# Performance work log

Hardware: AMD Instinct MI355X
Metric: run time of the kernel (lower is better)

## Reference

```python
import math
import jax, jax.numpy as jnp
import numpy as np

B, IMG, CIN = 32, 32, 4
PATCH, HIDDEN, DEPTH, HEADS, MLP = 2, 768, 12, 12, 3072
FREQ, NUM_CLASSES = 256, 1000
GRID = IMG // PATCH
N = GRID * GRID
OUT = PATCH * PATCH * CIN


def _pos_embed(dim, length):
    # faithful port of get_2d_sincos_pos_embed
    g = int(math.sqrt(length))
    grid = np.stack(np.meshgrid(np.arange(g, dtype=np.float32),
                                np.arange(g, dtype=np.float32), indexing='ij')).reshape(2, -1)
    def emb1d(d, pos):
        omega = 1.0 / 10000.0 ** (np.arange(d // 2, dtype=np.float32) / (d / 2.0))
        out = np.einsum('m,d->md', pos, omega)
        return np.concatenate([np.sin(out), np.cos(out)], axis=1)
    pe = np.concatenate([emb1d(dim // 2, grid[0]), emb1d(dim // 2, grid[1])], axis=1)
    return jnp.asarray(pe[None], dtype=jnp.float32)  # [1, N, dim]


def _ln(x):
    # LayerNorm(elementwise_affine=False), eps=1e-5, biased variance
    m = jnp.mean(x, axis=-1, keepdims=True)
    v = jnp.var(x, axis=-1, keepdims=True)
    return (x - m) * jax.lax.rsqrt(v + 1e-5)


def setup_inputs() -> dict:
    key = jax.random.key(0)
    ks = jax.random.split(key, 20)
    w = lambda k, shape: jax.random.normal(k, shape, jnp.float32) * 0.02
    z = lambda *shape: jnp.zeros(shape, jnp.float32)
    return {
        'x': jax.random.normal(ks[0], (B, IMG, IMG, CIN), jnp.float32),
        't': jax.random.uniform(ks[1], (B,), jnp.float32) * 1000.0,
        'y': jax.random.randint(ks[2], (B,), 0, NUM_CLASSES + 1),
        'patch_w': w(ks[3], (PATCH * PATCH * CIN, HIDDEN)), 'patch_b': z(HIDDEN),
        't_w1': w(ks[4], (FREQ, HIDDEN)), 't_b1': z(HIDDEN),
        't_w2': w(ks[5], (HIDDEN, HIDDEN)), 't_b2': z(HIDDEN),
        'label_emb': w(ks[6], (NUM_CLASSES + 1, HIDDEN)),
        'ada_w': w(ks[7], (DEPTH, HIDDEN, 6 * HIDDEN)), 'ada_b': z(DEPTH, 6 * HIDDEN),
        'q_w': w(ks[8], (DEPTH, HIDDEN, HIDDEN)), 'q_b': z(DEPTH, HIDDEN),
        'k_w': w(ks[9], (DEPTH, HIDDEN, HIDDEN)), 'k_b': z(DEPTH, HIDDEN),
        'v_w': w(ks[10], (DEPTH, HIDDEN, HIDDEN)), 'v_b': z(DEPTH, HIDDEN),
        'o_w': w(ks[11], (DEPTH, HIDDEN, HIDDEN)), 'o_b': z(DEPTH, HIDDEN),
        'fc1_w': w(ks[12], (DEPTH, HIDDEN, MLP)), 'fc1_b': z(DEPTH, MLP),
        'fc2_w': w(ks[13], (DEPTH, MLP, HIDDEN)), 'fc2_b': z(DEPTH, HIDDEN),
        'fin_ada_w': w(ks[14], (HIDDEN, 2 * HIDDEN)), 'fin_ada_b': z(2 * HIDDEN),
        'fin_w': w(ks[15], (HIDDEN, OUT)), 'fin_b': z(OUT),
    }


def reference(x, t, y, patch_w, patch_b, t_w1, t_b1, t_w2, t_b2, label_emb,
              ada_w, ada_b, q_w, q_b, k_w, k_b, v_w, v_b, o_w, o_b,
              fc1_w, fc1_b, fc2_w, fc2_b, fin_ada_w, fin_ada_b, fin_w, fin_b):
    Bx = x.shape[0]
    dh = HIDDEN // HEADS
    # patch embed (conv k=p, stride=p == per-patch linear)
    patches = x.reshape(Bx, GRID, PATCH, GRID, PATCH, CIN)
    patches = patches.transpose(0, 1, 3, 2, 4, 5).reshape(Bx, N, PATCH * PATCH * CIN)
    h = patches @ patch_w + patch_b + _pos_embed(HIDDEN, N)
    # timestep embedding: [cos, sin] order
    half = FREQ // 2
    freqs = jnp.exp(-math.log(10000.0) * jnp.arange(half, dtype=jnp.float32) / half)
    args = t.astype(jnp.float32)[:, None] * freqs[None]
    temb = jnp.concatenate([jnp.cos(args), jnp.sin(args)], axis=-1)
    temb = jax.nn.silu(temb @ t_w1 + t_b1) @ t_w2 + t_b2
    c_act = jax.nn.silu(temb + label_emb[y])  # silu applied inside each block on c

    def block(hx, p):
        aw, ab, qw, qb, kw, kb, vw, vb, ow, ob, f1w, f1b, f2w, f2b = p
        ada = c_act @ aw + ab
        sh_m, sc_m, g_m, sh_p, sc_p, g_p = jnp.split(ada, 6, axis=-1)
        xn = _ln(hx) * (1.0 + sc_m[:, None]) + sh_m[:, None]
        q = ((xn @ qw + qb).reshape(Bx, N, HEADS, dh)) / math.sqrt(3.0)
        k = (xn @ kw + kb).reshape(Bx, N, HEADS, dh)
        v = (xn @ vw + vb).reshape(Bx, N, HEADS, dh)
        attn = jax.nn.softmax(jnp.einsum('bqhc,bkhc->bhqk', q, k).astype(jnp.float32), axis=-1)
        yv = jnp.einsum('bhqk,bkhc->bqhc', attn, v).reshape(Bx, N, HIDDEN)
        hx = hx + g_m[:, None] * (yv @ ow + ob)
        xn2 = _ln(hx) * (1.0 + sc_p[:, None]) + sh_p[:, None]
        mlp = jax.nn.gelu(xn2 @ f1w + f1b, approximate=False) @ f2w + f2b
        hx = hx + g_p[:, None] * mlp
        return hx, None

    h, _ = jax.lax.scan(block, h, (ada_w, ada_b, q_w, q_b, k_w, k_b, v_w, v_b,
                                   o_w, o_b, fc1_w, fc1_b, fc2_w, fc2_b))
    # final layer
    fada = c_act @ fin_ada_w + fin_ada_b
    sh, sc = jnp.split(fada, 2, axis=-1)
    out = (_ln(h) * (1.0 + sc[:, None]) + sh[:, None]) @ fin_w + fin_b
    return out  # [B, N, patch*patch*out_channels]
```

## Files before the change

kernel.cpp:

```cpp
#include <hip/hip_runtime.h>
#include <hip/hip_bf16.h>


typedef short  s16x8 __attribute__((ext_vector_type(8)));
typedef float  f32x4 __attribute__((ext_vector_type(4)));

__device__ __forceinline__ float bf2f(unsigned short u) {
    union { unsigned int i; float f; } v; v.i = ((unsigned int)u) << 16; return v.f;
}
__device__ __forceinline__ unsigned short f2bf(float f) {
    union { float f; unsigned int i; } v; v.f = f;
    unsigned int r = (v.i + 0x7FFFu + ((v.i >> 16) & 1u)) >> 16;
    return (unsigned short)r;
}
__device__ __forceinline__ float silu(float v) { return v / (1.f + __expf(-v)); }

__device__ __forceinline__ void gload16(const void* gptr, void* lptr) {
    __builtin_amdgcn_global_load_lds(
        (const __attribute__((address_space(1))) unsigned int*)gptr,
        (__attribute__((address_space(3))) unsigned int*)lptr,
        16, 0, 0);
}

#define ROWS 8192
#define HID  768
#define MLPD 3072
#define ADA_LD 4608

__global__ __launch_bounds__(256) void ada_init(const float* __restrict__ ada_b,
                                                const float* __restrict__ fada_b,
                                                const float* __restrict__ t_b1,
                                                const float* __restrict__ t_b2,
                                                const float* __restrict__ lemb,
                                                const int* __restrict__ y,
                                                float* __restrict__ ada_all,
                                                float* __restrict__ fada,
                                                float* __restrict__ z1,
                                                float* __restrict__ z2)
{
    const int bid = blockIdx.x, tid = threadIdx.x;
    if (bid >= 222) {
        const int col = (bid - 222) * 256 + tid;
        const float b1v = t_b1[col], b2v = t_b2[col];
        for (int r = 0; r < 32; ++r) {
            z1[(size_t)r * HID + col] = b1v;
            z2[(size_t)r * HID + col] = b2v + lemb[(size_t)y[r] * HID + col];
        }
        return;
    }
    const float* Bv; float* Out; int ldw, colb;
    if (bid < 216) {
        const int l = bid / 18; colb = (bid % 18) * 256;
        Bv = ada_b + (size_t)l * ADA_LD; Out = ada_all + (size_t)l * 32 * ADA_LD; ldw = ADA_LD;
    } else {
        colb = (bid - 216) * 256;
        Bv = fada_b; Out = fada; ldw = 1536;
    }
    const int col = colb + tid;
    const float bb = Bv[col];
    #pragma unroll
    for (int r = 0; r < 32; ++r) Out[(size_t)r * ldw + col] = bb;
}

__global__ __launch_bounds__(256) void temb1_k(const float* __restrict__ t,
                                               const float* __restrict__ w1,
                                               float* __restrict__ z1)
{
    __shared__ float tin[128];
    const int b = blockIdx.x, cc = blockIdx.y, kc = blockIdx.z, tid = threadIdx.x;
    const int k0 = kc * 128;
    if (tid < 128) {
        const int k = k0 + tid, j = k & 127;
        const float fr = __expf((float)j * (-9.210340371976184f / 128.f));
        const float a = t[b] * fr;
        tin[tid] = (k < 128) ? cosf(a) : sinf(a);
    }
    __syncthreads();
    const int col = cc * 256 + tid;
    float acc = 0.f;
    #pragma unroll 8
    for (int kk = 0; kk < 128; ++kk) acc += tin[kk] * w1[(size_t)(k0 + kk) * HID + col];
    atomicAdd(&z1[(size_t)b * HID + col], acc);
}

__global__ __launch_bounds__(256) void temb2_k(const float* __restrict__ z1,
                                               const float* __restrict__ w2,
                                               float* __restrict__ z2)
{
    __shared__ float tin[192];
    const int b = blockIdx.x, cc = blockIdx.y, kc = blockIdx.z, tid = threadIdx.x;
    const int k0 = kc * 192;
    if (tid < 192) tin[tid] = silu(z1[(size_t)b * HID + k0 + tid]);
    __syncthreads();
    const int col = cc * 256 + tid;
    float acc = 0.f;
    #pragma unroll 8
    for (int kk = 0; kk < 192; ++kk) acc += tin[kk] * w2[(size_t)(k0 + kk) * HID + col];
    atomicAdd(&z2[(size_t)b * HID + col], acc);
}

__global__ __launch_bounds__(64) void ada_gemm2(const float* __restrict__ z2,
                                                const float* __restrict__ ada_w,
                                                const float* __restrict__ fada_w,
                                                float* __restrict__ ada_all,
                                                float* __restrict__ fada)
{
    const int bx = blockIdx.x, kc = blockIdx.y, tid = threadIdx.x;
    const float* W; float* Out; int ldw, colb;
    if (bx < 216) {
        const int l = bx / 18; colb = (bx % 18) * 256;
        W = ada_w + (size_t)l * HID * ADA_LD; Out = ada_all + (size_t)l * 32 * ADA_LD; ldw = ADA_LD;
    } else {
        colb = (bx - 216) * 256;
        W = fada_w; Out = fada; ldw = 1536;
    }
    const int k0 = kc * 96;
    __shared__ float cs_[32][96];
    for (int i = tid; i < 32 * 96; i += 64)
        cs_[i / 96][i % 96] = silu(z2[(size_t)(i / 96) * HID + k0 + (i % 96)]);
    __syncthreads();
    float acc[4][32];
    #pragma unroll
    for (int j = 0; j < 4; ++j)
        #pragma unroll
        for (int r = 0; r < 32; ++r) acc[j][r] = 0.f;
    #pragma unroll 1
    for (int kk = 0; kk < 96; kk += 4) {
        float wv[4][4];
        #pragma unroll
        for (int i = 0; i < 4; ++i) {
            const float* Wr = W + (size_t)(k0 + kk + i) * ldw + colb + tid;
            #pragma unroll
            for (int j = 0; j < 4; ++j) wv[j][i] = Wr[64 * j];
        }
        #pragma unroll
        for (int r = 0; r < 32; ++r) {
            const float4 cv = *(const float4*)&cs_[r][kk];
            #pragma unroll
            for (int j = 0; j < 4; ++j)
                acc[j][r] += cv.x * wv[j][0] + cv.y * wv[j][1] + cv.z * wv[j][2] + cv.w * wv[j][3];
        }
    }
    #pragma unroll
    for (int j = 0; j < 4; ++j)
        #pragma unroll
        for (int r = 0; r < 32; ++r)
            atomicAdd(&Out[(size_t)r * ldw + colb + tid + 64 * j], acc[j][r]);
}

__global__ __launch_bounds__(256) void patch_embed(const float* __restrict__ x,
                                                   const float* __restrict__ pw,
                                                   const float* __restrict__ pb,
                                                   float* __restrict__ h)
{
    const int row = blockIdx.x;
    const int b = row >> 8, n = row & 255;
    const int gi = n >> 4, gj = n & 15;
    const int tid = threadIdx.x;
    __shared__ float pv[16];
    if (tid < 16) {
        const int pr = tid >> 3, pc = (tid >> 2) & 1, ci = tid & 3;
        pv[tid] = x[((size_t)(b * 32 + gi * 2 + pr) * 32 + (gj * 2 + pc)) * 4 + ci];
    }
    __syncthreads();
    #pragma unroll
    for (int cc = 0; cc < 3; ++cc) {
        const int col = cc * 256 + tid;
        float acc = pb[col];
        #pragma unroll
        for (int i = 0; i < 16; ++i) acc += pv[i] * pw[(size_t)i * HID + col];
        const int d4 = (col < 384) ? col : col - 384;
        const int pos = (col < 384) ? gi : gj;
        const float kf = (float)(d4 < 192 ? d4 : d4 - 192);
        const float om = __expf(kf * (-9.210340371976184f / 192.f));
        const float a = (float)pos * om;
        acc += (d4 < 192) ? sinf(a) : cosf(a);
        h[(size_t)row * HID + col] = acc;
    }
}

__global__ __launch_bounds__(256) void convert_weights(
    const float* __restrict__ q_w, const float* __restrict__ k_w,
    const float* __restrict__ v_w, const float* __restrict__ o_w,
    const float* __restrict__ fc1_w, const float* __restrict__ fc2_w,
    const float* __restrict__ q_b, const float* __restrict__ k_b,
    const float* __restrict__ v_b,
    unsigned short* __restrict__ wbase, size_t slot_stride,
    float* __restrict__ cbias, int first_layer)
{
    const int bid = blockIdx.x;
    const int l = first_layer + bid / 6913;
    const int t = bid % 6913;
    unsigned short* dst = wbase + (size_t)(bid / 6913) * slot_stride;
    const int tid = threadIdx.x;
    if (t == 6912) {
        float* cb = cbias + (size_t)l * 2304;
        for (int i = tid; i < 2304; i += 256) {
            float v;
            if (i < 768)       v = q_b[(size_t)l * 768 + i];
            else if (i < 1536) v = k_b[(size_t)l * 768 + i - 768];
            else               v = v_b[(size_t)l * 768 + i - 1536];
            cb[i] = v;
        }
        return;
    }
    const float* src; int srcN; unsigned short* d; int dLd; int tr, tc;
    if (t < 2304) {
        const int mat = t / 576, tt = t % 576; tr = tt / 24; tc = tt % 24;
        srcN = 768; dLd = 768;
        if (mat == 0)      { src = q_w + (size_t)l * 589824; d = dst; }
        else if (mat == 1) { src = k_w + (size_t)l * 589824; d = dst + 589824; }
        else if (mat == 2) { src = v_w + (size_t)l * 589824; d = dst + 1179648; }
        else               { src = o_w + (size_t)l * 589824; d = dst + 1769472; }
    } else if (t < 4608) {
        const int tt = t - 2304; tr = tt / 96; tc = tt % 96;
        src = fc1_w + (size_t)l * 2359296; srcN = 3072; dLd = 768; d = dst + 2359296;
    } else {
        const int tt = t - 4608; tr = tt / 24; tc = tt % 24;
        src = fc2_w + (size_t)l * 2359296; srcN = 768; dLd = 3072; d = dst + 4718592;
    }
    __shared__ float lt[32][33];
    const int tx = tid & 31, ty = tid >> 5;
    const int r0 = tr * 32, c0 = tc * 32;
    #pragma unroll
    for (int i = 0; i < 4; ++i)
        lt[ty + i * 8][tx] = src[(size_t)(r0 + ty + i * 8) * srcN + c0 + tx];
    __syncthreads();
    #pragma unroll
    for (int i = 0; i < 4; ++i)
        d[(size_t)(c0 + ty + i * 8) * dLd + r0 + tx] = f2bf(lt[tx][ty + i * 8]);
}

__global__ __launch_bounds__(192) void ln_mod(const float* __restrict__ hbuf,
                                              const float* __restrict__ mod,
                                              int sh_off, int sc_off, int mld,
                                              unsigned short* __restrict__ xout)
{
    const int row = blockIdx.x, tid = threadIdx.x;
    const float4 xv = *(const float4*)&hbuf[(size_t)row * HID + tid * 4];
    float s = (xv.x + xv.y) + (xv.z + xv.w);
    float ss = (xv.x * xv.x + xv.y * xv.y) + (xv.z * xv.z + xv.w * xv.w);
    #pragma unroll
    for (int d = 1; d < 64; d <<= 1) { s += __shfl_xor(s, d); ss += __shfl_xor(ss, d); }
    __shared__ float sb[3], ssb[3];
    if ((tid & 63) == 0) { sb[tid >> 6] = s; ssb[tid >> 6] = ss; }
    __syncthreads();
    s = sb[0] + sb[1] + sb[2];
    ss = ssb[0] + ssb[1] + ssb[2];
    const float mean = s * (1.f / 768.f);
    const float var = ss * (1.f / 768.f) - mean * mean;
    const float rs = rsqrtf(var + 1e-5f);
    const int b = row >> 8;
    const float* mrow = mod + (size_t)b * mld;
    const float4 sc = *(const float4*)&mrow[sc_off + tid * 4];
    const float4 sh = *(const float4*)&mrow[sh_off + tid * 4];
    ushort4 o;
    o.x = f2bf((xv.x - mean) * rs * (1.f + sc.x) + sh.x);
    o.y = f2bf((xv.y - mean) * rs * (1.f + sc.y) + sh.y);
    o.z = f2bf((xv.z - mean) * rs * (1.f + sc.z) + sh.z);
    o.w = f2bf((xv.w - mean) * rs * (1.f + sc.w) + sh.w);
    *(ushort4*)&xout[(size_t)row * HID + tid * 4] = o;
}

template<int EPI, int BN>
__global__ __launch_bounds__(256) void gemm_bt(const unsigned short* __restrict__ A,
                                               const unsigned short* __restrict__ Bt,
                                               const float* __restrict__ bias,
                                               void* __restrict__ outp,
                                               const float* __restrict__ gate,
                                               int K, int ldo)
{
    constexpr int BELEMS = BN * 32;
    constexpr int NJ = BN / 32;
    __shared__ unsigned short sAB[2][4096 + BELEMS];
    const int tid = threadIdx.x;
    const int lane = tid & 63;
    const int w = tid >> 6;
    const int wm = w >> 1, wn = w & 1;
    const int rowbase = blockIdx.y << 7;
    const int colbase = blockIdx.x * BN;
    const size_t a0 = (size_t)(rowbase +      (tid >> 2)) * K + (tid & 3) * 8;
    const size_t a1 = (size_t)(rowbase + 64 + (tid >> 2)) * K + (tid & 3) * 8;
    const size_t b0 = (size_t)(colbase +      (tid >> 2)) * K + (tid & 3) * 8;
    size_t b1 = 0;
    if constexpr (BN == 128)
        b1 = (size_t)(colbase + 64 + (tid >> 2)) * K + (tid & 3) * 8;
    const int ldsw = w * 512;
    f32x4 acc[4][NJ];
    #pragma unroll
    for (int i = 0; i < 4; ++i)
        #pragma unroll
        for (int j = 0; j < NJ; ++j) acc[i][j] = (f32x4){0.f, 0.f, 0.f, 0.f};
    const int nk = K >> 5;
    const int lm = lane & 15, lg = lane >> 4;
    {
        unsigned short* base = &sAB[0][0];
        gload16(A + a0,  base + ldsw);
        gload16(A + a1,  base + 2048 + ldsw);
        gload16(Bt + b0, base + 4096 + ldsw);
        if constexpr (BN == 128) gload16(Bt + b1, base + 6144 + ldsw);
    }
    __syncthreads();
    int cur = 0;
    for (int kt = 0; kt < nk; ++kt) {
        if (kt + 1 < nk) {
            const int k0 = (kt + 1) << 5;
            unsigned short* base = &sAB[cur ^ 1][0];
            gload16(A + a0 + k0,  base + ldsw);
            gload16(A + a1 + k0,  base + 2048 + ldsw);
            gload16(Bt + b0 + k0, base + 4096 + ldsw);
            if constexpr (BN == 128) gload16(Bt + b1 + k0, base + 6144 + ldsw);
        }
        const unsigned short* sAc = &sAB[cur][0];
        const unsigned short* sBc = &sAB[cur][4096];
        s16x8 af[4], bfr[NJ];
        #pragma unroll
        for (int mi = 0; mi < 4; ++mi)
            af[mi] = *(const s16x8*)&sAc[(wm * 64 + mi * 16 + lm) * 32 + lg * 8];
        #pragma unroll
        for (int nj = 0; nj < NJ; ++nj)
            bfr[nj] = *(const s16x8*)&sBc[(wn * (16 * NJ) + nj * 16 + lm) * 32 + lg * 8];
        #pragma unroll
        for (int mi = 0; mi < 4; ++mi)
            #pragma unroll
            for (int nj = 0; nj < NJ; ++nj)
                acc[mi][nj] = __builtin_amdgcn_mfma_f32_16x16x32_bf16(af[mi], bfr[nj], acc[mi][nj], 0, 0, 0);
        __syncthreads();
        cur ^= 1;
    }
    float bv[NJ], gv[NJ];
    #pragma unroll
    for (int nj = 0; nj < NJ; ++nj) {
        const int col = colbase + wn * (16 * NJ) + nj * 16 + lm;
        bv[nj] = bias[col];
        if constexpr (EPI == 2) gv[nj] = gate[(size_t)(rowbase >> 8) * ADA_LD + col];
    }
    #pragma unroll
    for (int mi = 0; mi < 4; ++mi) {
        const int row = rowbase + wm * 64 + mi * 16 + (lg << 2);
        #pragma unroll
        for (int nj = 0; nj < NJ; ++nj) {
            const int col = colbase + wn * (16 * NJ) + nj * 16 + lm;
            #pragma unroll
            for (int r = 0; r < 4; ++r) {
                const float v = acc[mi][nj][r] + bv[nj];
                if constexpr (EPI == 0) {
                    ((unsigned short*)outp)[(size_t)(row + r) * ldo + col] = f2bf(v);
                } else if constexpr (EPI == 1) {
                    const float g = 0.5f * v * (1.f + erff(v * 0.70710678118654752f));
                    ((unsigned short*)outp)[(size_t)(row + r) * ldo + col] = f2bf(g);
                } else {
                    float* O = (float*)outp;
                    const size_t idx = (size_t)(row + r) * ldo + col;
                    O[idx] = O[idx] + gv[nj] * v;
                }
            }
        }
    }
}

__global__ __launch_bounds__(256) void attn_fused(const unsigned short* __restrict__ qkv,
                                                  unsigned short* __restrict__ yv)
{
    __shared__ unsigned short Vt[64][264];
    __shared__ unsigned short Psm[4][32 * 72];
    __shared__ float Ssc[4][32];
    const int bid = blockIdx.x;
    const int b = bid / 24, rem = bid % 24, h = rem >> 1, half = rem & 1;
    const int tid = threadIdx.x, w = tid >> 6, lane = tid & 63;
    {
        const int dhg = tid & 7, tk = tid >> 3;
        #pragma unroll
        for (int g = 0; g < 8; ++g) {
            const int tok = tk + g * 32;
            s16x8 vv = *(const s16x8*)(qkv + (size_t)(b * 256 + tok) * 2304 + 1536 + h * 64 + dhg * 8);
            #pragma unroll
            for (int j = 0; j < 8; ++j) Vt[dhg * 8 + j][tok] = (unsigned short)vv[j];
        }
    }
    __syncthreads();
    const int q0 = half * 128 + w * 32;
    const int lm = lane & 15, lg = lane >> 4;
    const unsigned short* Qb = qkv + (size_t)(b * 256 + q0) * 2304 + h * 64;
    s16x8 qf[2][2];
    #pragma unroll
    for (int ni = 0; ni < 2; ++ni)
        #pragma unroll
        for (int kk = 0; kk < 2; ++kk)
            qf[ni][kk] = *(const s16x8*)(Qb + (size_t)(ni * 16 + lm) * 2304 + kk * 32 + lg * 8);
    f32x4 o_[2][4];
    #pragma unroll
    for (int i = 0; i < 2; ++i)
        #pragma unroll
        for (int j = 0; j < 4; ++j) o_[i][j] = (f32x4){0.f, 0.f, 0.f, 0.f};
    float m_[2], l_[2];
    #pragma unroll
    for (int i = 0; i < 2; ++i) { m_[i] = -1e30f; l_[i] = 0.f; }
    const float s3 = 0.57735026918962576f;
    for (int c = 0; c < 4; ++c) {
        f32x4 st[4][2];
        #pragma unroll
        for (int i = 0; i < 4; ++i)
            #pragma unroll
            for (int j = 0; j < 2; ++j) st[i][j] = (f32x4){0.f, 0.f, 0.f, 0.f};
        const unsigned short* Kb = qkv + (size_t)(b * 256 + c * 64) * 2304 + 768 + h * 64;
        __builtin_amdgcn_s_setprio(1);
        #pragma unroll
        for (int kk = 0; kk < 2; ++kk)
            #pragma unroll
            for (int mi = 0; mi < 4; ++mi) {
                const s16x8 kf = *(const s16x8*)(Kb + (size_t)(mi * 16 + lm) * 2304 + kk * 32 + lg * 8);
                #pragma unroll
                for (int ni = 0; ni < 2; ++ni)
                    st[mi][ni] = __builtin_amdgcn_mfma_f32_16x16x32_bf16(kf, qf[ni][kk], st[mi][ni], 0, 0, 0);
            }
        __builtin_amdgcn_s_setprio(0);
        #pragma unroll
        for (int ni = 0; ni < 2; ++ni) {
            float cm = -1e30f;
            #pragma unroll
            for (int mi = 0; mi < 4; ++mi)
                #pragma unroll
                for (int r = 0; r < 4; ++r) cm = fmaxf(cm, st[mi][ni][r]);
            cm = fmaxf(cm, __shfl_xor(cm, 16));
            cm = fmaxf(cm, __shfl_xor(cm, 32));
            cm *= s3;
            const float mn = fmaxf(m_[ni], cm);
            const float corr = __expf(m_[ni] - mn);
            float cs = 0.f;
            #pragma unroll
            for (int mi = 0; mi < 4; ++mi) {
                float p0 = __expf(st[mi][ni][0] * s3 - mn);
                float p1 = __expf(st[mi][ni][1] * s3 - mn);
                float p2 = __expf(st[mi][ni][2] * s3 - mn);
                float p3 = __expf(st[mi][ni][3] * s3 - mn);
                cs += (p0 + p1) + (p2 + p3);
                uint2 pk;
                pk.x = (unsigned int)f2bf(p0) | ((unsigned int)f2bf(p1) << 16);
                pk.y = (unsigned int)f2bf(p2) | ((unsigned int)f2bf(p3) << 16);
                *(uint2*)&Psm[w][(ni * 16 + lm) * 72 + mi * 16 + lg * 4] = pk;
            }
            cs += __shfl_xor(cs, 16);
            cs += __shfl_xor(cs, 32);
            l_[ni] = l_[ni] * corr + cs;
            m_[ni] = mn;
            if (lane < 16) Ssc[w][ni * 16 + lane] = corr;
        }
        asm volatile("" ::: "memory");
        #pragma unroll
        for (int qi = 0; qi < 2; ++qi) {
            float fr[4];
            #pragma unroll
            for (int r = 0; r < 4; ++r) fr[r] = Ssc[w][qi * 16 + lg * 4 + r];
            #pragma unroll
            for (int di = 0; di < 4; ++di)
                #pragma unroll
                for (int r = 0; r < 4; ++r) o_[qi][di][r] *= fr[r];
        }
        __builtin_amdgcn_s_setprio(1);
        #pragma unroll
        for (int kk = 0; kk < 2; ++kk)
            #pragma unroll
            for (int qi = 0; qi < 2; ++qi) {
                const s16x8 pa = *(const s16x8*)&Psm[w][(qi * 16 + lm) * 72 + kk * 32 + lg * 8];
                #pragma unroll
                for (int di = 0; di < 4; ++di) {
                    const s16x8 vb = *(const s16x8*)&Vt[di * 16 + lm][c * 64 + kk * 32 + lg * 8];
                    o_[qi][di] = __builtin_amdgcn_mfma_f32_16x16x32_bf16(pa, vb, o_[qi][di], 0, 0, 0);
                }
            }
        __builtin_amdgcn_s_setprio(0);
    }
    asm volatile("" ::: "memory");
    if (lane < 16) {
        #pragma unroll
        for (int ni = 0; ni < 2; ++ni) Ssc[w][ni * 16 + lane] = 1.f / l_[ni];
    }
    asm volatile("" ::: "memory");
    #pragma unroll
    for (int qi = 0; qi < 2; ++qi) {
        float fr[4];
        #pragma unroll
        for (int r = 0; r < 4; ++r) fr[r] = Ssc[w][qi * 16 + lg * 4 + r];
        #pragma unroll
        for (int di = 0; di < 4; ++di)
            #pragma unroll
            for (int r = 0; r < 4; ++r) {
                const float val = o_[qi][di][r] * fr[r];
                yv[(size_t)(b * 256 + q0 + qi * 16 + lg * 4 + r) * HID + h * 64 + di * 16 + lm] = f2bf(val);
            }
    }
}

__global__ __launch_bounds__(256) void fin_gemm(const unsigned short* __restrict__ xn,
                                                const float* __restrict__ w,
                                                const float* __restrict__ bias,
                                                float* __restrict__ out)
{
    __shared__ unsigned short xs[16 * 768];
    const int rb = blockIdx.x * 16, tid = threadIdx.x;
    #pragma unroll
    for (int i = 0; i < 6; ++i) {
        const int v = tid + i * 256;
        const int row = v / 96, koff = (v % 96) * 8;
        *(s16x8*)&xs[v * 8] = *(const s16x8*)(xn + (size_t)(rb + row) * HID + koff);
    }
    __syncthreads();
    const int r = tid >> 4, o = tid & 15;
    float acc = bias[o];
    #pragma unroll 8
    for (int k = 0; k < 768; ++k) acc += bf2f(xs[r * 768 + k]) * w[(size_t)k * 16 + o];
    out[(size_t)(rb + r) * 16 + o] = acc;
}

extern "C" void kernel_launch(void* const* d_in, const int* in_sizes, int n_in,
                              void* d_out, int out_size, void* d_ws, size_t ws_size,
                              hipStream_t stream)
{
    const float* x        = (const float*)d_in[0];
    const float* t        = (const float*)d_in[1];
    const int*   y        = (const int*)d_in[2];
    const float* patch_w  = (const float*)d_in[3];
    const float* patch_b  = (const float*)d_in[4];
    const float* t_w1     = (const float*)d_in[5];
    const float* t_b1     = (const float*)d_in[6];
    const float* t_w2     = (const float*)d_in[7];
    const float* t_b2     = (const float*)d_in[8];
    const float* label_e  = (const float*)d_in[9];
    const float* ada_w    = (const float*)d_in[10];
    const float* ada_b    = (const float*)d_in[11];
    const float* q_w      = (const float*)d_in[12];
    const float* q_b      = (const float*)d_in[13];
    const float* k_w      = (const float*)d_in[14];
    const float* k_b      = (const float*)d_in[15];
    const float* v_w      = (const float*)d_in[16];
    const float* v_b      = (const float*)d_in[17];
    const float* o_w      = (const float*)d_in[18];
    const float* o_b      = (const float*)d_in[19];
    const float* fc1_w    = (const float*)d_in[20];
    const float* fc1_b    = (const float*)d_in[21];
    const float* fc2_w    = (const float*)d_in[22];
    const float* fc2_b    = (const float*)d_in[23];
    const float* fada_w   = (const float*)d_in[24];
    const float* fada_b   = (const float*)d_in[25];
    const float* fin_w    = (const float*)d_in[26];
    const float* fin_b    = (const float*)d_in[27];

    char* ws = (char*)d_ws;
    size_t off = 0;
    auto alloc = [&](size_t bytes) { size_t o = off; off = (off + bytes + 255) & ~(size_t)255; return o; };
    const size_t OFF_H    = alloc((size_t)ROWS * HID * 4);
    const size_t OFF_XN   = alloc((size_t)ROWS * HID * 2);
    const size_t OFF_QKV  = alloc((size_t)ROWS * 2304 * 2);
    const size_t OFF_YV   = alloc((size_t)ROWS * HID * 2);
    const size_t OFF_MLP  = alloc((size_t)ROWS * MLPD * 2);
    const size_t OFF_ADA  = alloc((size_t)12 * 32 * ADA_LD * 4);
    const size_t OFF_FADA = alloc((size_t)32 * 1536 * 4);
    const size_t OFF_Z2   = alloc((size_t)32 * HID * 4);
    const size_t OFF_Z1   = alloc((size_t)32 * HID * 4);
    const size_t OFF_CB   = alloc((size_t)12 * 2304 * 4);
    const size_t OFF_W    = off;
    const size_t WSLOT_ELEMS = 7077888;
    const bool big = (ws_size >= OFF_W + (size_t)12 * WSLOT_ELEMS * 2);

    float*          h     = (float*)(ws + OFF_H);
    unsigned short* xn    = (unsigned short*)(ws + OFF_XN);
    unsigned short* qkv   = (unsigned short*)(ws + OFF_QKV);
    unsigned short* yv    = (unsigned short*)(ws + OFF_YV);
    unsigned short* mlp   = (unsigned short*)(ws + OFF_MLP);
    float*          adaA  = (float*)(ws + OFF_ADA);
    float*          fada  = (float*)(ws + OFF_FADA);
    float*          z2    = (float*)(ws + OFF_Z2);
    float*          z1    = (float*)(ws + OFF_Z1);
    float*          cbias = (float*)(ws + OFF_CB);
    unsigned short* wsW   = (unsigned short*)(ws + OFF_W);

    ada_init<<<225, 256, 0, stream>>>(ada_b, fada_b, t_b1, t_b2, label_e, y,
                                      adaA, fada, z1, z2);
    temb1_k<<<dim3(32, 3, 2), 256, 0, stream>>>(t, t_w1, z1);
    temb2_k<<<dim3(32, 3, 4), 256, 0, stream>>>(z1, t_w2, z2);
    ada_gemm2<<<dim3(222, 8), 64, 0, stream>>>(z2, ada_w, fada_w, adaA, fada);
    patch_embed<<<8192, 256, 0, stream>>>(x, patch_w, patch_b, h);
    if (big) {
        convert_weights<<<6913 * 12, 256, 0, stream>>>(q_w, k_w, v_w, o_w, fc1_w, fc2_w,
                                                       q_b, k_b, v_b, wsW, WSLOT_ELEMS, cbias, 0);
    }

    for (int l = 0; l < 12; ++l) {
        unsigned short* wslot = wsW + (big ? (size_t)l * WSLOT_ELEMS : 0);
        if (!big) {
            convert_weights<<<6913, 256, 0, stream>>>(q_w, k_w, v_w, o_w, fc1_w, fc2_w,
                                                      q_b, k_b, v_b, wslot, 0, cbias, l);
        }
        unsigned short* qkvT = wslot;
        unsigned short* oT   = wslot + 1769472;
        unsigned short* f1T  = wslot + 2359296;
        unsigned short* f2T  = wslot + 4718592;
        float* ada_l  = adaA + (size_t)l * 32 * ADA_LD;
        float* cb_l   = cbias + (size_t)l * 2304;

        ln_mod<<<8192, 192, 0, stream>>>(h, ada_l, 0, 768, ADA_LD, xn);
        gemm_bt<0, 128><<<dim3(18, 64), 256, 0, stream>>>(xn, qkvT, cb_l, qkv, nullptr, 768, 2304);
        attn_fused<<<768, 256, 0, stream>>>(qkv, yv);
        gemm_bt<2, 64><<<dim3(12, 64), 256, 0, stream>>>(yv, oT, o_b + (size_t)l * 768, h,
                                                         ada_l + 1536, 768, 768);
        ln_mod<<<8192, 192, 0, stream>>>(h, ada_l, 2304, 3072, ADA_LD, xn);
        gemm_bt<1, 128><<<dim3(24, 64), 256, 0, stream>>>(xn, f1T, fc1_b + (size_t)l * 3072, mlp,
                                                          nullptr, 768, 3072);
        gemm_bt<2, 64><<<dim3(12, 64), 256, 0, stream>>>(mlp, f2T, fc2_b + (size_t)l * 768, h,
                                                         ada_l + 3840, 3072, 768);
    }

    ln_mod<<<8192, 192, 0, stream>>>(h, fada, 0, 768, 1536, xn);
    fin_gemm<<<512, 256, 0, stream>>>(xn, fin_w, fin_b, (float*)d_out);
}
```

Baseline: 3.550 ms.

## Swizzle GEMM workgroup order, widen ada GEMM blocks, pack bf16 transpose stores

The bf16 GEMM now remaps linear workgroup IDs so consecutive groups of eight are spread across the tile grid. This is aimed at improving L2 / cross-XCD locality of A and B tiles. The adaLN modulation GEMM moves from 64 threads handling four columns each to 256 threads handling one column each, which cuts register pressure and raises occupancy. The weight conversion transpose writes two bf16 values per 32-bit store instead of single 16-bit stores. The swizzle assumes the grid size is a multiple of eight.

```diff
diff --git a/kernel.cpp b/kernel.cpp
--- a/kernel.cpp
+++ b/kernel.cpp
@@ -99,11 +99,11 @@
     atomicAdd(&z2[(size_t)b * HID + col], acc);
 }
 
-__global__ __launch_bounds__(64) void ada_gemm2(const float* __restrict__ z2,
-                                                const float* __restrict__ ada_w,
-                                                const float* __restrict__ fada_w,
-                                                float* __restrict__ ada_all,
-                                                float* __restrict__ fada)
+__global__ __launch_bounds__(256) void ada_gemm2(const float* __restrict__ z2,
+                                                 const float* __restrict__ ada_w,
+                                                 const float* __restrict__ fada_w,
+                                                 float* __restrict__ ada_all,
+                                                 float* __restrict__ fada)
 {
     const int bx = blockIdx.x, kc = blockIdx.y, tid = threadIdx.x;
     const float* W; float* Out; int ldw, colb;
@@ -114,38 +114,29 @@
         colb = (bx - 216) * 256;
         W = fada_w; Out = fada; ldw = 1536;
     }
+    const int col = colb + tid;
     const int k0 = kc * 96;
     __shared__ float cs_[32][96];
-    for (int i = tid; i < 32 * 96; i += 64)
+    for (int i = tid; i < 32 * 96; i += 256)
         cs_[i / 96][i % 96] = silu(z2[(size_t)(i / 96) * HID + k0 + (i % 96)]);
     __syncthreads();
-    float acc[4][32];
-    #pragma unroll
-    for (int j = 0; j < 4; ++j)
-        #pragma unroll
-        for (int r = 0; r < 32; ++r) acc[j][r] = 0.f;
-    #pragma unroll 1
+    float acc[32];
+    #pragma unroll
+    for (int r = 0; r < 32; ++r) acc[r] = 0.f;
+    #pragma unroll 2
     for (int kk = 0; kk < 96; kk += 4) {
-        float wv[4][4];
-        #pragma unroll
-        for (int i = 0; i < 4; ++i) {
-            const float* Wr = W + (size_t)(k0 + kk + i) * ldw + colb + tid;
-            #pragma unroll
-            for (int j = 0; j < 4; ++j) wv[j][i] = Wr[64 * j];
-        }
+        const float w0 = W[(size_t)(k0 + kk) * ldw + col];
+        const float w1 = W[(size_t)(k0 + kk + 1) * ldw + col];
+        const float w2 = W[(size_t)(k0 + kk + 2) * ldw + col];
+        const float w3 = W[(size_t)(k0 + kk + 3) * ldw + col];
         #pragma unroll
         for (int r = 0; r < 32; ++r) {
             const float4 cv = *(const float4*)&cs_[r][kk];
-            #pragma unroll
-            for (int j = 0; j < 4; ++j)
-                acc[j][r] += cv.x * wv[j][0] + cv.y * wv[j][1] + cv.z * wv[j][2] + cv.w * wv[j][3];
-        }
-    }
-    #pragma unroll
-    for (int j = 0; j < 4; ++j)
-        #pragma unroll
-        for (int r = 0; r < 32; ++r)
-            atomicAdd(&Out[(size_t)r * ldw + colb + tid + 64 * j], acc[j][r]);
+            acc[r] += cv.x * w0 + cv.y * w1 + cv.z * w2 + cv.w * w3;
+        }
+    }
+    #pragma unroll
+    for (int r = 0; r < 32; ++r) atomicAdd(&Out[(size_t)r * ldw + col], acc[r]);
 }
 
 __global__ __launch_bounds__(256) void patch_embed(const float* __restrict__ x,
@@ -226,9 +217,15 @@
     for (int i = 0; i < 4; ++i)
         lt[ty + i * 8][tx] = src[(size_t)(r0 + ty + i * 8) * srcN + c0 + tx];
     __syncthreads();
-    #pragma unroll
-    for (int i = 0; i < 4; ++i)
-        d[(size_t)(c0 + ty + i * 8) * dLd + r0 + tx] = f2bf(lt[tx][ty + i * 8]);
+    const int q = tid & 15;
+    const int cw = tid >> 4;
+    #pragma unroll
+    for (int i = 0; i < 2; ++i) {
+        const int cc = cw + i * 16;
+        const unsigned int pk = (unsigned int)f2bf(lt[2 * q][cc])
+                              | ((unsigned int)f2bf(lt[2 * q + 1][cc]) << 16);
+        *(unsigned int*)&d[(size_t)(c0 + cc) * dLd + r0 + 2 * q] = pk;
+    }
 }
 
 __global__ __launch_bounds__(192) void ln_mod(const float* __restrict__ hbuf,
@@ -277,8 +274,12 @@
     const int lane = tid & 63;
     const int w = tid >> 6;
     const int wm = w >> 1, wn = w & 1;
-    const int rowbase = blockIdx.y << 7;
-    const int colbase = blockIdx.x * BN;
+    const int nwg = gridDim.x * gridDim.y;
+    int bidl = blockIdx.y * gridDim.x + blockIdx.x;
+    bidl = (bidl & 7) * (nwg >> 3) + (bidl >> 3);
+    const int bx = bidl % gridDim.x, by = bidl / gridDim.x;
+    const int rowbase = by << 7;
+    const int colbase = bx * BN;
     const size_t a0 = (size_t)(rowbase +      (tid >> 2)) * K + (tid & 3) * 8;
     const size_t a1 = (size_t)(rowbase + 64 + (tid >> 2)) * K + (tid & 3) * 8;
     const size_t b0 = (size_t)(colbase +      (tid >> 2)) * K + (tid & 3) * 8;
@@ -579,7 +580,7 @@
                                       adaA, fada, z1, z2);
     temb1_k<<<dim3(32, 3, 2), 256, 0, stream>>>(t, t_w1, z1);
     temb2_k<<<dim3(32, 3, 4), 256, 0, stream>>>(z1, t_w2, z2);
-    ada_gemm2<<<dim3(222, 8), 64, 0, stream>>>(z2, ada_w, fada_w, adaA, fada);
+    ada_gemm2<<<dim3(222, 8), 256, 0, stream>>>(z2, ada_w, fada_w, adaA, fada);
     patch_embed<<<8192, 256, 0, stream>>>(x, patch_w, patch_b, h);
     if (big) {
         convert_weights<<<6913 * 12, 256, 0, stream>>>(q_w, k_w, v_w, o_w, fc1_w, fc2_w,
```

After: 3.414 ms. -3.8%, faster.
